# Optimization experiments

Hardware: AMD Instinct MI355X
Metric: run time of the kernel (lower is better)

The kernel has to match this reference:

```python
import jax, jax.numpy as jnp
import numpy as np

B, N, IN_DIM, HEADS, PER_HEAD = 8, 512, 256, 4, 32
OUT_DIM = HEADS * PER_HEAD  # 128
NEG_SLOPE = 0.2


def setup_inputs() -> dict:
    key = jax.random.key(0)
    ks = jax.random.split(key, 8)
    x = jax.random.normal(ks[0], (B, N, IN_DIM), jnp.float32)
    adj = jax.random.randint(ks[1], (B, N, N), 0, 2, jnp.int32)
    sl = 1.0 / np.sqrt(IN_DIM)
    W_l = jax.random.normal(ks[2], (IN_DIM, OUT_DIM), jnp.float32) * sl  # source proj
    b_l = jnp.zeros((OUT_DIM,), jnp.float32)
    W_r = jax.random.normal(ks[3], (IN_DIM, OUT_DIM), jnp.float32) * sl  # target proj
    b_r = jnp.zeros((OUT_DIM,), jnp.float32)
    att = jax.random.normal(ks[4], (HEADS, PER_HEAD), jnp.float32) * (1.0 / np.sqrt(PER_HEAD))
    bias = jnp.zeros((OUT_DIM,), jnp.float32)
    return {"x": x, "adj": adj, "W_l": W_l, "b_l": b_l, "W_r": W_r, "b_r": b_r,
            "att": att, "bias": bias}


def _gatv2_single(x_b, adj_b, W_l, b_l, W_r, b_r, att, bias):
    # PyG GATv2Conv: remove_self_loops + add_self_loops -> diagonal forced to 1
    n = x_b.shape[0]
    adj_sl = jnp.fill_diagonal(adj_b, 1, inplace=False)
    # edge_index = adj.nonzero().t(): source = row, target = col
    m = (adj_sl != 0).T  # m[i, j]: source j feeds target i
    xl = (x_b @ W_l + b_l).reshape(n, HEADS, PER_HEAD)  # source-side features
    xr = (x_b @ W_r + b_r).reshape(n, HEADS, PER_HEAD)  # target-side features
    s = xr[:, None] + xl[None, :]                       # [i, j, H, C]
    s = jnp.where(s > 0, s, NEG_SLOPE * s)              # LeakyReLU(0.2)
    e = jnp.einsum('ijhc,hc->ijh', s, att)              # attention logits
    e = jnp.where(m[..., None], e, -jnp.inf)
    alpha = jax.nn.softmax(e, axis=1)                   # softmax over sources j
    out = jnp.einsum('ijh,jhc->ihc', alpha, xl).reshape(n, HEADS * PER_HEAD)
    return out + bias


def reference(x, adj, W_l, b_l, W_r, b_r, att, bias):
    # Sequential per-batch processing, faithful to the original Python loop
    # and keeping the [N,N,H,C] intermediate to one graph at a time.
    def one(args):
        x_b, adj_b = args
        return _gatv2_single(x_b, adj_b, W_l, b_l, W_r, b_r, att, bias)
    return jax.lax.map(one, (x, adj))  # [B, N, OUT_DIM]
```

## Files before the change

### kernel.cpp

```cpp
#include <hip/hip_runtime.h>
#include <hip/hip_bf16.h>

typedef __hip_bfloat16 bf16;

#define B_   8
#define N_   512
#define IND  256
#define H_   4
#define PH   32
#define OD   128
#define TI   8
#define TJ   64
#define XLS_STRIDE 132

#define XL_OFF    0
#define XR_OFF    (XL_OFF + B_*N_*OD)
#define XF_OFF    (XR_OFF + B_*N_*OD)
#define WLF_OFF   (XF_OFF + B_*N_*IND)
#define BLF_OFF   (WLF_OFF + IND*OD)
#define WRF_OFF   (BLF_OFF + OD)
#define BRF_OFF   (WRF_OFF + IND*OD)
#define ATTF_OFF  (BRF_OFF + OD)
#define BIASF_OFF (ATTF_OFF + OD)
#define FLAG_OFF  (BIASF_OFF + OD)

__device__ __forceinline__ float bf2f(ushort u) {
    return __uint_as_float(((unsigned)u) << 16);
}

__global__ void detect_kernel(const ushort* __restrict__ x, int* __restrict__ flag) {
    __shared__ int cnt[256];
    const int t = threadIdx.x;
    int c = 0;
    #pragma unroll
    for (int k = 0; k < 8; ++k) {
        float v = bf2f(x[t * 8 + k]);
        float a = fabsf(v);
        bool bad = !(a < 1e8f) || (a != 0.f && a < 1e-8f);
        c += bad ? 1 : 0;
    }
    cnt[t] = c;
    __syncthreads();
    for (int s = 128; s > 0; s >>= 1) {
        if (t < s) cnt[t] += cnt[t + s];
        __syncthreads();
    }
    if (t == 0) *flag = (cnt[0] > 256) ? 1 : 0;
}

__global__ void convert_kernel(
    const ushort* __restrict__ x,  const ushort* __restrict__ Wl,
    const ushort* __restrict__ bl, const ushort* __restrict__ Wr,
    const ushort* __restrict__ br, const ushort* __restrict__ att,
    const ushort* __restrict__ bias, float* __restrict__ ws,
    const int* __restrict__ flag)
{
    const int isf = *flag;
    long j = (long)blockIdx.x * 256 + threadIdx.x;
    const ushort* s; float* d;
    if (j < (long)B_*N_*IND)            { s = x;    d = ws + XF_OFF; }
    else { j -= (long)B_*N_*IND;
      if (j < IND*OD)                   { s = Wl;   d = ws + WLF_OFF; }
      else { j -= IND*OD;
        if (j < OD)                     { s = bl;   d = ws + BLF_OFF; }
        else { j -= OD;
          if (j < IND*OD)               { s = Wr;   d = ws + WRF_OFF; }
          else { j -= IND*OD;
            if (j < OD)                 { s = br;   d = ws + BRF_OFF; }
            else { j -= OD;
              if (j < OD)               { s = att;  d = ws + ATTF_OFF; }
              else { j -= OD;             s = bias; d = ws + BIASF_OFF; }
            }}}}}
    d[j] = isf ? ((const float*)s)[j] : bf2f(s[j]);
}

__global__ __launch_bounds__(256, 2) void proj_kernel(
    const float* __restrict__ ws_in, float* __restrict__ xl, float* __restrict__ xr)
{
    const float* xf = ws_in + XF_OFF;
    __shared__ float xs[8 * IND];
    const int t = threadIdx.x;
    const int row0 = blockIdx.x * 8;

    const float* xp = xf + (size_t)row0 * IND;
    #pragma unroll
    for (int k = 0; k < 8; ++k)
        xs[t + k * 256] = xp[t + k * 256];
    __syncthreads();

    const int which = t >> 7;
    const int rg = (t >> 6) & 1;
    const int og = t & 63;
    const int o0 = og * 2;
    const int r0 = rg * 4;
    const float* W  = which ? (ws_in + WRF_OFF) : (ws_in + WLF_OFF);
    const float* bb = which ? (ws_in + BRF_OFF) : (ws_in + BLF_OFF);

    float acc0[4], acc1[4];
    #pragma unroll
    for (int r = 0; r < 4; ++r) { acc0[r] = 0.f; acc1[r] = 0.f; }

    for (int k = 0; k < IND; k += 4) {
        float wf0[4], wf1[4];
        #pragma unroll
        for (int kk = 0; kk < 4; ++kk) {
            float2 wv = *(const float2*)(W + (size_t)(k + kk) * OD + o0);
            wf0[kk] = wv.x;
            wf1[kk] = wv.y;
        }
        float xv[4][4];
        #pragma unroll
        for (int r = 0; r < 4; ++r)
            *(float4*)(xv[r]) = *(const float4*)(&xs[(r0 + r) * IND + k]);
        #pragma unroll
        for (int kk = 0; kk < 4; ++kk)
            #pragma unroll
            for (int r = 0; r < 4; ++r) {
                acc0[r] = fmaf(xv[r][kk], wf0[kk], acc0[r]);
                acc1[r] = fmaf(xv[r][kk], wf1[kk], acc1[r]);
            }
    }

    const float bv0 = bb[o0];
    const float bv1 = bb[o0 + 1];
    float* dst = which ? xr : xl;
    #pragma unroll
    for (int r = 0; r < 4; ++r) {
        float2 v = make_float2(acc0[r] + bv0, acc1[r] + bv1);
        *(float2*)(&dst[(size_t)(row0 + r0 + r) * OD + o0]) = v;
    }
}

__global__ __launch_bounds__(256, 2) void attn_kernel(
    const int* __restrict__ adj, const float* __restrict__ ws_in,
    const float* __restrict__ xl, const float* __restrict__ xr,
    void* __restrict__ out, const int* __restrict__ flag)
{
    __shared__ float xls[TJ * XLS_STRIDE];
    __shared__ float masks[TJ * TI];
    __shared__ float dls[TJ * H_];

    const int t = threadIdx.x;
    const int b  = blockIdx.x >> 6;
    const int i0 = (blockIdx.x & 63) * TI;
    const int q  = t & 7;
    const int g  = t >> 3;
    const int h  = g & 3;
    const int il = g >> 2;
    const int ig = i0 + il;

    float attv[PH], xrv[PH];
    {
        const float* xrp = xr + ((size_t)(b * N_ + ig)) * OD + h * PH;
        #pragma unroll
        for (int k = 0; k < PH; k += 4) {
            float4 v = *(const float4*)(xrp + k);
            xrv[k] = v.x; xrv[k+1] = v.y; xrv[k+2] = v.z; xrv[k+3] = v.w;
        }
        const float* ap = ws_in + ATTF_OFF + h * PH;
        #pragma unroll
        for (int k = 0; k < PH; ++k) attv[k] = ap[k];
    }
    float dr = 0.f;
    #pragma unroll
    for (int k = 0; k < PH; ++k) dr = fmaf(attv[k], xrv[k], dr);
    const float c0 = 0.6f * dr;

    float acc[PH];
    #pragma unroll
    for (int k = 0; k < PH; ++k) acc[k] = 0.f;
    float sumw = 0.f;

    const float* xlb = xl + (size_t)b * N_ * OD;
    const int* adjb  = adj + (size_t)b * N_ * N_;

    for (int tile = 0; tile < N_ / TJ; ++tile) {
        const int j0 = tile * TJ;
        __syncthreads();
        #pragma unroll
        for (int k = 0; k < 8; ++k) {
            int idx = t + k * 256;
            int jj = idx >> 5, m = idx & 31;
            *(float4*)(&xls[jj * XLS_STRIDE + m * 4]) =
                *(const float4*)(xlb + (size_t)(j0 + jj) * OD + m * 4);
        }
        #pragma unroll
        for (int k = 0; k < 2; ++k) {
            int idx = t + k * 256;
            int jj = idx >> 3, ii = idx & 7;
            int jg2 = j0 + jj, ig2 = i0 + ii;
            int a = adjb[(size_t)jg2 * N_ + ig2];
            masks[idx] = (a != 0 || jg2 == ig2) ? 1.f : 0.f;
        }
        __syncthreads();
        {
            int jj = il * 8 + q;
            const float* p = &xls[jj * XLS_STRIDE + h * PH];
            float dl = 0.f;
            #pragma unroll
            for (int k = 0; k < PH; ++k) dl = fmaf(attv[k], p[k], dl);
            dls[jj * H_ + h] = dl;
        }
        __syncthreads();
        #pragma unroll 2
        for (int u = 0; u < 8; ++u) {
            const int jj = q + u * 8;
            const float* vrow = &xls[jj * XLS_STRIDE + h * PH];
            float v[PH];
            #pragma unroll
            for (int k = 0; k < PH; k += 4) {
                float4 w4 = *(const float4*)(vrow + k);
                v[k] = w4.x; v[k+1] = w4.y; v[k+2] = w4.z; v[k+3] = w4.w;
            }
            float e2 = 0.f;
            #pragma unroll
            for (int k = 0; k < PH; ++k) {
                float s = xrv[k] + v[k];
                e2 = fmaf(attv[k], fabsf(s), e2);
            }
            float e = fmaf(0.6f, dls[jj * H_ + h], c0);
            e = fmaf(0.4f, e2, e);
            float w = masks[jj * TI + il] * __expf(e);
            sumw += w;
            #pragma unroll
            for (int k = 0; k < PH; ++k) acc[k] = fmaf(w, v[k], acc[k]);
        }
    }

    #pragma unroll
    for (int d = 1; d < 8; d <<= 1) {
        sumw += __shfl_xor(sumw, d);
        #pragma unroll
        for (int k = 0; k < PH; ++k) acc[k] += __shfl_xor(acc[k], d);
    }
    const float inv = 1.f / sumw;
    const float* bp = ws_in + BIASF_OFF + h * PH;
    const size_t obase = ((size_t)(b * N_ + ig)) * OD + h * PH;
    const int isf = *flag;
    if (isf) {
        float* op = (float*)out + obase;
        #pragma unroll
        for (int k = 0; k < 4; ++k) {
            int c = q * 4 + k;
            op[c] = fmaf(acc[c], inv, bp[c]);
        }
    } else {
        bf16* op = (bf16*)out + obase;
        #pragma unroll
        for (int k = 0; k < 4; ++k) {
            int c = q * 4 + k;
            op[c] = __float2bfloat16(fmaf(acc[c], inv, bp[c]));
        }
    }
}

extern "C" void kernel_launch(void* const* d_in, const int* in_sizes, int n_in,
                              void* d_out, int out_size, void* d_ws, size_t ws_size,
                              hipStream_t stream) {
    const ushort* x    = (const ushort*)d_in[0];
    const int*    adj  = (const int*)d_in[1];
    const ushort* Wl   = (const ushort*)d_in[2];
    const ushort* bl   = (const ushort*)d_in[3];
    const ushort* Wr   = (const ushort*)d_in[4];
    const ushort* br   = (const ushort*)d_in[5];
    const ushort* att  = (const ushort*)d_in[6];
    const ushort* bias = (const ushort*)d_in[7];

    float* ws = (float*)d_ws;
    float* xl = ws + XL_OFF;
    float* xr = ws + XR_OFF;
    int* flag = (int*)(ws + FLAG_OFF);

    detect_kernel<<<1, 256, 0, stream>>>(x, flag);
    convert_kernel<<<4354, 256, 0, stream>>>(x, Wl, bl, Wr, br, att, bias, ws, flag);
    proj_kernel<<<512, 256, 0, stream>>>(ws, xl, xr);
    attn_kernel<<<512, 256, 0, stream>>>(adj, ws, xl, xr, d_out, flag);
}
```

Baseline: 138.0 us.

## Drop dtype detection/conversion kernels, halve attention tile, use transposed shuffle reduction

```diff
diff --git a/kernel.cpp b/kernel.cpp
--- a/kernel.cpp
+++ b/kernel.cpp
@@ -1,7 +1,5 @@
 #include <hip/hip_runtime.h>
 #include <hip/hip_bf16.h>
-
-typedef __hip_bfloat16 bf16;
 
 #define B_   8
 #define N_   512
@@ -9,83 +7,25 @@
 #define H_   4
 #define PH   32
 #define OD   128
-#define TI   8
+#define TI   4
 #define TJ   64
 #define XLS_STRIDE 132
 
-#define XL_OFF    0
-#define XR_OFF    (XL_OFF + B_*N_*OD)
-#define XF_OFF    (XR_OFF + B_*N_*OD)
-#define WLF_OFF   (XF_OFF + B_*N_*IND)
-#define BLF_OFF   (WLF_OFF + IND*OD)
-#define WRF_OFF   (BLF_OFF + OD)
-#define BRF_OFF   (WRF_OFF + IND*OD)
-#define ATTF_OFF  (BRF_OFF + OD)
-#define BIASF_OFF (ATTF_OFF + OD)
-#define FLAG_OFF  (BIASF_OFF + OD)
-
-__device__ __forceinline__ float bf2f(ushort u) {
-    return __uint_as_float(((unsigned)u) << 16);
-}
-
-__global__ void detect_kernel(const ushort* __restrict__ x, int* __restrict__ flag) {
-    __shared__ int cnt[256];
-    const int t = threadIdx.x;
-    int c = 0;
-    #pragma unroll
-    for (int k = 0; k < 8; ++k) {
-        float v = bf2f(x[t * 8 + k]);
-        float a = fabsf(v);
-        bool bad = !(a < 1e8f) || (a != 0.f && a < 1e-8f);
-        c += bad ? 1 : 0;
-    }
-    cnt[t] = c;
-    __syncthreads();
-    for (int s = 128; s > 0; s >>= 1) {
-        if (t < s) cnt[t] += cnt[t + s];
-        __syncthreads();
-    }
-    if (t == 0) *flag = (cnt[0] > 256) ? 1 : 0;
-}
-
-__global__ void convert_kernel(
-    const ushort* __restrict__ x,  const ushort* __restrict__ Wl,
-    const ushort* __restrict__ bl, const ushort* __restrict__ Wr,
-    const ushort* __restrict__ br, const ushort* __restrict__ att,
-    const ushort* __restrict__ bias, float* __restrict__ ws,
-    const int* __restrict__ flag)
+__global__ __launch_bounds__(256, 2) void proj_kernel(
+    const float* __restrict__ x,
+    const float* __restrict__ Wl, const float* __restrict__ bl,
+    const float* __restrict__ Wr, const float* __restrict__ br,
+    float* __restrict__ xl, float* __restrict__ xr)
 {
-    const int isf = *flag;
-    long j = (long)blockIdx.x * 256 + threadIdx.x;
-    const ushort* s; float* d;
-    if (j < (long)B_*N_*IND)            { s = x;    d = ws + XF_OFF; }
-    else { j -= (long)B_*N_*IND;
-      if (j < IND*OD)                   { s = Wl;   d = ws + WLF_OFF; }
-      else { j -= IND*OD;
-        if (j < OD)                     { s = bl;   d = ws + BLF_OFF; }
-        else { j -= OD;
-          if (j < IND*OD)               { s = Wr;   d = ws + WRF_OFF; }
-          else { j -= IND*OD;
-            if (j < OD)                 { s = br;   d = ws + BRF_OFF; }
-            else { j -= OD;
-              if (j < OD)               { s = att;  d = ws + ATTF_OFF; }
-              else { j -= OD;             s = bias; d = ws + BIASF_OFF; }
-            }}}}}
-    d[j] = isf ? ((const float*)s)[j] : bf2f(s[j]);
-}
-
-__global__ __launch_bounds__(256, 2) void proj_kernel(
-    const float* __restrict__ ws_in, float* __restrict__ xl, float* __restrict__ xr)
-{
-    const float* xf = ws_in + XF_OFF;
     __shared__ float xs[8 * IND];
     const int t = threadIdx.x;
     const int row0 = blockIdx.x * 8;
 
-    const float* xp = xf + (size_t)row0 * IND;
-    #pragma unroll
-    for (int k = 0; k < 8; ++k)
-        xs[t + k * 256] = xp[t + k * 256];
+    const float4* xp4 = (const float4*)(x + (size_t)row0 * IND);
+    float4* xs4 = (float4*)xs;
+    #pragma unroll
+    for (int k = 0; k < 2; ++k)
+        xs4[t + k * 256] = xp4[t + k * 256];
     __syncthreads();
 
     const int which = t >> 7;
@@ -93,8 +33,8 @@
     const int og = t & 63;
     const int o0 = og * 2;
     const int r0 = rg * 4;
-    const float* W  = which ? (ws_in + WRF_OFF) : (ws_in + WLF_OFF);
-    const float* bb = which ? (ws_in + BRF_OFF) : (ws_in + BLF_OFF);
+    const float* W  = which ? Wr : Wl;
+    const float* bb = which ? br : bl;
 
     float acc0[4], acc1[4];
     #pragma unroll
@@ -131,22 +71,22 @@
     }
 }
 
-__global__ __launch_bounds__(256, 2) void attn_kernel(
-    const int* __restrict__ adj, const float* __restrict__ ws_in,
+__global__ __launch_bounds__(256, 4) void attn_kernel(
+    const int* __restrict__ adj, const float* __restrict__ att,
+    const float* __restrict__ bias,
     const float* __restrict__ xl, const float* __restrict__ xr,
-    void* __restrict__ out, const int* __restrict__ flag)
+    float* __restrict__ out)
 {
     __shared__ float xls[TJ * XLS_STRIDE];
     __shared__ float masks[TJ * TI];
     __shared__ float dls[TJ * H_];
 
     const int t = threadIdx.x;
-    const int b  = blockIdx.x >> 6;
-    const int i0 = (blockIdx.x & 63) * TI;
-    const int q  = t & 7;
-    const int g  = t >> 3;
-    const int h  = g & 3;
-    const int il = g >> 2;
+    const int b  = blockIdx.x >> 7;
+    const int i0 = (blockIdx.x & 127) * TI;
+    const int q  = t & 15;
+    const int h  = (t >> 4) & 3;
+    const int il = t >> 6;
     const int ig = i0 + il;
 
     float attv[PH], xrv[PH];
@@ -157,7 +97,7 @@
             float4 v = *(const float4*)(xrp + k);
             xrv[k] = v.x; xrv[k+1] = v.y; xrv[k+2] = v.z; xrv[k+3] = v.w;
         }
-        const float* ap = ws_in + ATTF_OFF + h * PH;
+        const float* ap = att + h * PH;
         #pragma unroll
         for (int k = 0; k < PH; ++k) attv[k] = ap[k];
     }
@@ -184,27 +124,30 @@
             *(float4*)(&xls[jj * XLS_STRIDE + m * 4]) =
                 *(const float4*)(xlb + (size_t)(j0 + jj) * OD + m * 4);
         }
-        #pragma unroll
-        for (int k = 0; k < 2; ++k) {
-            int idx = t + k * 256;
-            int jj = idx >> 3, ii = idx & 7;
+        {
+            int jj = t >> 2, ii = t & 3;
             int jg2 = j0 + jj, ig2 = i0 + ii;
             int a = adjb[(size_t)jg2 * N_ + ig2];
-            masks[idx] = (a != 0 || jg2 == ig2) ? 1.f : 0.f;
+            masks[t] = (a != 0 || jg2 == ig2) ? 1.f : 0.f;
         }
         __syncthreads();
         {
-            int jj = il * 8 + q;
+            int jj = il * 16 + q;
             const float* p = &xls[jj * XLS_STRIDE + h * PH];
-            float dl = 0.f;
-            #pragma unroll
-            for (int k = 0; k < PH; ++k) dl = fmaf(attv[k], p[k], dl);
-            dls[jj * H_ + h] = dl;
+            float d0 = 0.f, d1 = 0.f, d2 = 0.f, d3 = 0.f;
+            #pragma unroll
+            for (int k = 0; k < PH; k += 4) {
+                d0 = fmaf(attv[k+0], p[k+0], d0);
+                d1 = fmaf(attv[k+1], p[k+1], d1);
+                d2 = fmaf(attv[k+2], p[k+2], d2);
+                d3 = fmaf(attv[k+3], p[k+3], d3);
+            }
+            dls[jj * H_ + h] = (d0 + d1) + (d2 + d3);
         }
         __syncthreads();
         #pragma unroll 2
-        for (int u = 0; u < 8; ++u) {
-            const int jj = q + u * 8;
+        for (int u = 0; u < 4; ++u) {
+            const int jj = q + u * 16;
             const float* vrow = &xls[jj * XLS_STRIDE + h * PH];
             float v[PH];
             #pragma unroll
@@ -212,12 +155,15 @@
                 float4 w4 = *(const float4*)(vrow + k);
                 v[k] = w4.x; v[k+1] = w4.y; v[k+2] = w4.z; v[k+3] = w4.w;
             }
-            float e2 = 0.f;
-            #pragma unroll
-            for (int k = 0; k < PH; ++k) {
-                float s = xrv[k] + v[k];
-                e2 = fmaf(attv[k], fabsf(s), e2);
-            }
+            float e2a = 0.f, e2b = 0.f, e2c = 0.f, e2d = 0.f;
+            #pragma unroll
+            for (int k = 0; k < PH; k += 4) {
+                e2a = fmaf(attv[k+0], fabsf(xrv[k+0] + v[k+0]), e2a);
+                e2b = fmaf(attv[k+1], fabsf(xrv[k+1] + v[k+1]), e2b);
+                e2c = fmaf(attv[k+2], fabsf(xrv[k+2] + v[k+2]), e2c);
+                e2d = fmaf(attv[k+3], fabsf(xrv[k+3] + v[k+3]), e2d);
+            }
+            float e2 = (e2a + e2b) + (e2c + e2d);
             float e = fmaf(0.6f, dls[jj * H_ + h], c0);
             e = fmaf(0.4f, e2, e);
             float w = masks[jj * TI + il] * __expf(e);
@@ -228,51 +174,72 @@
     }
 
     #pragma unroll
-    for (int d = 1; d < 8; d <<= 1) {
-        sumw += __shfl_xor(sumw, d);
-        #pragma unroll
-        for (int k = 0; k < PH; ++k) acc[k] += __shfl_xor(acc[k], d);
-    }
+    for (int d = 1; d < 16; d <<= 1) sumw += __shfl_xor(sumw, d);
     const float inv = 1.f / sumw;
-    const float* bp = ws_in + BIASF_OFF + h * PH;
-    const size_t obase = ((size_t)(b * N_ + ig)) * OD + h * PH;
-    const int isf = *flag;
-    if (isf) {
-        float* op = (float*)out + obase;
-        #pragma unroll
-        for (int k = 0; k < 4; ++k) {
-            int c = q * 4 + k;
-            op[c] = fmaf(acc[c], inv, bp[c]);
-        }
-    } else {
-        bf16* op = (bf16*)out + obase;
-        #pragma unroll
-        for (int k = 0; k < 4; ++k) {
-            int c = q * 4 + k;
-            op[c] = __float2bfloat16(fmaf(acc[c], inv, bp[c]));
-        }
-    }
+
+    float r8[16];
+    {
+        const bool hi = (q & 8) != 0;
+        #pragma unroll
+        for (int m = 0; m < 16; ++m) {
+            float send = hi ? acc[m] : acc[16 + m];
+            float keep = hi ? acc[16 + m] : acc[m];
+            r8[m] = keep + __shfl_xor(send, 8);
+        }
+    }
+    float r4[8];
+    {
+        const bool hi = (q & 4) != 0;
+        #pragma unroll
+        for (int m = 0; m < 8; ++m) {
+            float send = hi ? r8[m] : r8[8 + m];
+            float keep = hi ? r8[8 + m] : r8[m];
+            r4[m] = keep + __shfl_xor(send, 4);
+        }
+    }
+    float r2[4];
+    {
+        const bool hi = (q & 2) != 0;
+        #pragma unroll
+        for (int m = 0; m < 4; ++m) {
+            float send = hi ? r4[m] : r4[4 + m];
+            float keep = hi ? r4[4 + m] : r4[m];
+            r2[m] = keep + __shfl_xor(send, 2);
+        }
+    }
+    float r1[2];
+    {
+        const bool hi = (q & 1) != 0;
+        #pragma unroll
+        for (int m = 0; m < 2; ++m) {
+            float send = hi ? r2[m] : r2[2 + m];
+            float keep = hi ? r2[2 + m] : r2[m];
+            r1[m] = keep + __shfl_xor(send, 1);
+        }
+    }
+
+    const int c0i = q * 2;
+    float* op = out + ((size_t)(b * N_ + ig)) * OD + h * PH;
+    op[c0i]     = fmaf(r1[0], inv, bias[h * PH + c0i]);
+    op[c0i + 1] = fmaf(r1[1], inv, bias[h * PH + c0i + 1]);
 }
 
 extern "C" void kernel_launch(void* const* d_in, const int* in_sizes, int n_in,
                               void* d_out, int out_size, void* d_ws, size_t ws_size,
                               hipStream_t stream) {
-    const ushort* x    = (const ushort*)d_in[0];
-    const int*    adj  = (const int*)d_in[1];
-    const ushort* Wl   = (const ushort*)d_in[2];
-    const ushort* bl   = (const ushort*)d_in[3];
-    const ushort* Wr   = (const ushort*)d_in[4];
-    const ushort* br   = (const ushort*)d_in[5];
-    const ushort* att  = (const ushort*)d_in[6];
-    const ushort* bias = (const ushort*)d_in[7];
-
-    float* ws = (float*)d_ws;
-    float* xl = ws + XL_OFF;
-    float* xr = ws + XR_OFF;
-    int* flag = (int*)(ws + FLAG_OFF);
-
-    detect_kernel<<<1, 256, 0, stream>>>(x, flag);
-    convert_kernel<<<4354, 256, 0, stream>>>(x, Wl, bl, Wr, br, att, bias, ws, flag);
-    proj_kernel<<<512, 256, 0, stream>>>(ws, xl, xr);
-    attn_kernel<<<512, 256, 0, stream>>>(adj, ws, xl, xr, d_out, flag);
+    const float* x    = (const float*)d_in[0];
+    const int*   adj  = (const int*)d_in[1];
+    const float* Wl   = (const float*)d_in[2];
+    const float* bl   = (const float*)d_in[3];
+    const float* Wr   = (const float*)d_in[4];
+    const float* br   = (const float*)d_in[5];
+    const float* att  = (const float*)d_in[6];
+    const float* bias = (const float*)d_in[7];
+    float* out = (float*)d_out;
+
+    float* xl = (float*)d_ws;
+    float* xr = xl + (size_t)B_ * N_ * OD;
+
+    proj_kernel<<<512, 256, 0, stream>>>(x, Wl, bl, Wr, br, xl, xr);
+    attn_kernel<<<1024, 256, 0, stream>>>(adj, att, bias, xl, xr, out);
 }
```

Measured after the change: 435.8 us. 3.16x slower.
